# Performance work log

Hardware: AMD Instinct MI355X
Metric: run time of the kernel (lower is better)

## Reference

```python
import jax, jax.numpy as jnp
import numpy as np

C = 512
CR = C // 8  # reduced channels for b/c projections


def setup_inputs() -> dict:
    key = jax.random.key(0)
    ks = jax.random.split(key, 7)
    scale = 1.0 / np.sqrt(C)
    x = jax.random.normal(ks[0], (4, C, 64, 64), dtype=jnp.float32)
    Wb = jax.random.normal(ks[1], (CR, C), dtype=jnp.float32) * scale
    bb = jax.random.normal(ks[2], (CR,), dtype=jnp.float32) * 0.01
    Wc = jax.random.normal(ks[3], (CR, C), dtype=jnp.float32) * scale
    bc = jax.random.normal(ks[4], (CR,), dtype=jnp.float32) * 0.01
    Wd = jax.random.normal(ks[5], (C, C), dtype=jnp.float32) * scale
    bd = jax.random.normal(ks[6], (C,), dtype=jnp.float32) * 0.01
    return {"x": x, "Wb": Wb, "bb": bb, "Wc": Wc, "bc": bc, "Wd": Wd, "bd": bd}


def reference(x, Wb, bb, Wc, bc, Wd, bd):
    B, Cc, H, W = x.shape
    N = H * W
    xf = x.reshape(B, Cc, N)  # [B, C, N] (1x1 conv == per-position matmul)
    b = jnp.einsum('kc,bcn->bkn', Wb, xf) + bb[None, :, None]  # [B, CR, N]
    c = jnp.einsum('kc,bcn->bkn', Wc, xf) + bc[None, :, None]  # [B, CR, N]
    d = jnp.einsum('kc,bcn->bkn', Wd, xf) + bd[None, :, None]  # [B, C, N]
    # s[b,i,j] = sum_k b[b,k,i] * c[b,k,j]; softmax over j
    s = jnp.einsum('bki,bkj->bij', b, c)  # [B, N, N]
    s = jax.nn.softmax(s, axis=-1)
    # torch.bmm(d, s): y[b,c,j] = sum_i d[b,c,i] * s[b,i,j]
    y = jnp.einsum('bci,bij->bcj', d, s)  # [B, C, N]
    return x + y.reshape(B, Cc, H, W)
```

## Files before the change

kernel.cpp:

```cpp
#include <hip/hip_runtime.h>
#include <hip/hip_bf16.h>

typedef float f32x4 __attribute__((ext_vector_type(4)));
typedef float f32x16 __attribute__((ext_vector_type(16)));
typedef short s16x8 __attribute__((ext_vector_type(8)));
typedef uint  u32x4 __attribute__((ext_vector_type(4)));

#define MFMA_BF16(a, b, c) __builtin_amdgcn_mfma_f32_16x16x32_bf16((a), (b), (c), 0, 0, 0)
#define MFMA32(a, b, c)    __builtin_amdgcn_mfma_f32_32x32x16_bf16((a), (b), (c), 0, 0, 0)

__device__ __forceinline__ ushort f2bf(float f) {
  uint u = __builtin_bit_cast(uint, f);
  u += 0x7FFFu + ((u >> 16) & 1u);
  return (ushort)(u >> 16);
}
__device__ __forceinline__ uint pack2bf(float a, float b) {
  return (uint)f2bf(a) | ((uint)f2bf(b) << 16);
}
__device__ __forceinline__ float pexp(float s) {
  float t = fmaf(s, 1.4426950408889634f, -43.2808512266689f);
  float r;
  asm("v_exp_f32 %0, %1" : "=v"(r) : "v"(t));
  return r;
}
__device__ __forceinline__ uint cvtpk(float lo, float hi) {
  uint r;
  asm("v_cvt_pk_bf16_f32 %0, %1, %2" : "=v"(r) : "v"(lo), "v"(hi));
  return r;
}
__device__ __forceinline__ void plswap(uint& a, uint& b) {
  asm("v_permlane32_swap_b32 %0, %1" : "+v"(a), "+v"(b));
}
__device__ __forceinline__ void gld16(const void* g, void* l) {
  __builtin_amdgcn_global_load_lds(
      (const __attribute__((address_space(1))) unsigned int*)g,
      (__attribute__((address_space(3))) unsigned int*)l, 16, 0, 0);
}

#define WS_XT    0UL
#define WS_D     16777216UL
#define WS_BT    33554432UL
#define WS_CT    35651584UL
#define WS_WCAT  37748736UL
#define WS_BCAT  38404096UL
#define WS_E     41943040UL
#define WS_E_NEED (WS_E + 134217728UL)

__global__ void k_prep_w(const float* __restrict__ Wb, const float* __restrict__ bb,
                         const float* __restrict__ Wc, const float* __restrict__ bc,
                         const float* __restrict__ Wd, const float* __restrict__ bd,
                         ushort* __restrict__ Wcat, float* __restrict__ bcat) {
  int idx = blockIdx.x * 256 + threadIdx.x;
  if (idx < 640 * 512) {
    int m = idx >> 9, k = idx & 511;
    float v = (m < 64) ? Wb[m * 512 + k] : (m < 128) ? Wc[(m - 64) * 512 + k] : Wd[(m - 128) * 512 + k];
    Wcat[idx] = f2bf(v);
  }
  if (idx < 640) {
    bcat[idx] = (idx < 64) ? bb[idx] : (idx < 128) ? bc[idx - 64] : bd[idx - 128];
  }
}

__global__ __launch_bounds__(256) void k_prep_xt(const float* __restrict__ x, ushort* __restrict__ xT) {
  __shared__ float tile[64][65];
  int bx = blockIdx.x;
  int b = bx >> 9;
  int c0 = ((bx >> 6) & 7) * 64;
  int n0 = (bx & 63) * 64;
  int t = threadIdx.x;
  const float* xb = x + (size_t)b * 512 * 4096;
#pragma unroll
  for (int p = 0; p < 4; ++p) {
    int cl = (t >> 4) + 16 * p;
    int nf = (t & 15) * 4;
    float4 v = *reinterpret_cast<const float4*>(xb + (size_t)(c0 + cl) * 4096 + n0 + nf);
    tile[cl][nf + 0] = v.x; tile[cl][nf + 1] = v.y; tile[cl][nf + 2] = v.z; tile[cl][nf + 3] = v.w;
  }
  __syncthreads();
  ushort* dst = xT + (size_t)b * 4096 * 512;
#pragma unroll
  for (int q = 0; q < 2; ++q) {
    int ch = t + 256 * q;
    int nl = ch >> 3;
    int cf = (ch & 7) * 8;
    uint4 o;
    o.x = pack2bf(tile[cf + 0][nl], tile[cf + 1][nl]);
    o.y = pack2bf(tile[cf + 2][nl], tile[cf + 3][nl]);
    o.z = pack2bf(tile[cf + 4][nl], tile[cf + 5][nl]);
    o.w = pack2bf(tile[cf + 6][nl], tile[cf + 7][nl]);
    *reinterpret_cast<uint4*>(dst + (size_t)(n0 + nl) * 512 + c0 + cf) = o;
  }
}

__global__ __launch_bounds__(256) void k_proj(const ushort* __restrict__ Wcat, const float* __restrict__ bcat,
                                              const ushort* __restrict__ xT, ushort* __restrict__ bT,
                                              ushort* __restrict__ cT, ushort* __restrict__ dmat) {
  int bx = blockIdx.x;
  int b = bx / 160;
  int r = bx % 160;
  int m0 = (r >> 5) * 128;
  int n0 = (r & 31) * 128;
  int t = threadIdx.x, l = t & 63, w = t >> 6;
  int wm = w >> 1, wn = w & 1, g = l >> 4, l15 = l & 15;
  const ushort* xb = xT + (size_t)b * 4096 * 512;
  f32x4 acc[4][4] = {};
  s16x8 bfn[4];
#pragma unroll
  for (int nt = 0; nt < 4; ++nt)
    bfn[nt] = *reinterpret_cast<const s16x8*>(xb + (size_t)(n0 + 64 * wn + 16 * nt + l15) * 512 + 8 * g);
  for (int k0 = 0; k0 < 512; k0 += 32) {
    s16x8 a[4], bf[4];
#pragma unroll
    for (int nt = 0; nt < 4; ++nt) bf[nt] = bfn[nt];
#pragma unroll
    for (int mt = 0; mt < 4; ++mt)
      a[mt] = *reinterpret_cast<const s16x8*>(Wcat + (size_t)(m0 + 64 * wm + 16 * mt + l15) * 512 + k0 + 8 * g);
    if (k0 + 32 < 512) {
#pragma unroll
      for (int nt = 0; nt < 4; ++nt)
        bfn[nt] = *reinterpret_cast<const s16x8*>(xb + (size_t)(n0 + 64 * wn + 16 * nt + l15) * 512 + k0 + 32 + 8 * g);
    }
    __builtin_amdgcn_sched_barrier(0);
#pragma unroll
    for (int mt = 0; mt < 4; ++mt)
#pragma unroll
      for (int nt = 0; nt < 4; ++nt)
        acc[mt][nt] = MFMA_BF16(a[mt], bf[nt], acc[mt][nt]);
  }
#pragma unroll
  for (int mt = 0; mt < 4; ++mt) {
    int mbase = m0 + 64 * wm + 16 * mt + 4 * g;
#pragma unroll
    for (int nt = 0; nt < 4; ++nt) {
      int n = n0 + 64 * wn + 16 * nt + l15;
      float vv[4];
      vv[0] = acc[mt][nt][0] + bcat[mbase + 0];
      vv[1] = acc[mt][nt][1] + bcat[mbase + 1];
      vv[2] = acc[mt][nt][2] + bcat[mbase + 2];
      vv[3] = acc[mt][nt][3] + bcat[mbase + 3];
      if (mbase < 64) {
        uint2 u2; u2.x = pack2bf(vv[0], vv[1]); u2.y = pack2bf(vv[2], vv[3]);
        size_t off = ((size_t)b * 4096 + n) * 64 + (size_t)((((mbase >> 3) ^ (n & 7)) << 3) + (mbase & 4));
        *reinterpret_cast<uint2*>(bT + off) = u2;
      } else if (mbase < 128) {
        uint2 u2; u2.x = pack2bf(vv[0], vv[1]); u2.y = pack2bf(vv[2], vv[3]);
        *reinterpret_cast<uint2*>(cT + ((size_t)b * 4096 + n) * 64 + (mbase - 64)) = u2;
      } else {
        int cc = mbase - 128;
        size_t fb = (((size_t)b * 256 + (n >> 4)) * 16) * 512;
#pragma unroll
        for (int rr = 0; rr < 4; ++rr) {
          int c = cc + rr;
          size_t idx = fb + (size_t)(c >> 5) * 512 + (size_t)(((n >> 3) & 1) * 32 + (c & 31)) * 8 + (n & 7);
          dmat[idx] = f2bf(vv[rr]);
        }
      }
    }
  }
}

__global__ __launch_bounds__(512) void k_stats_e(const ushort* __restrict__ bT, const ushort* __restrict__ cT,
                                                 ushort* __restrict__ dmat, ushort* __restrict__ E) {
  __shared__ ushort sCT[3][8192];
  __shared__ float lsum[64];
  int bx = blockIdx.x;
  int b = bx >> 6;
  int IC = bx & 63;
  int i0 = IC * 64;
  int t = threadIdx.x, w = t >> 6, l = t & 63;
  int l31 = l & 31, hi = l >> 5;
  int it_s = w & 1, Jl = w >> 1;
  if (t < 64) lsum[t] = 0.f;
  const ushort* bTb = bT + (size_t)b * 262144;
  const ushort* cTb = cT + (size_t)b * 262144;
  int ri = i0 + 32 * it_s + l31;
  int r7 = ri & 7;
  s16x8 af[4];
#pragma unroll
  for (int kc = 0; kc < 4; ++kc)
    af[kc] = *reinterpret_cast<const s16x8*>(bTb + (size_t)ri * 64 + (((2 * kc + hi) ^ r7) << 3));
  __builtin_amdgcn_sched_barrier(0);
  auto STAGE = [&](int st) {
#pragma unroll
    for (int q = 0; q < 2; ++q) {
      int idx = t + 512 * q;
      int row = idx >> 3, u = idx & 7;
      gld16(cTb + (size_t)(st * 128 + row) * 64 + ((u ^ (row & 7)) << 3), &sCT[st % 3][idx * 8]);
    }
  };
  STAGE(0); STAGE(1);
  asm volatile("s_waitcnt vmcnt(2)" ::: "memory");
  __syncthreads();

  f32x16 zero16;
#pragma unroll
  for (int r = 0; r < 16; ++r) zero16[r] = 0.f;
  float lacc[16];
#pragma unroll
  for (int r = 0; r < 16; ++r) lacc[r] = 0.f;

  for (int st = 0; st < 32; ++st) {
    if (st + 2 < 32) STAGE(st + 2);
    __builtin_amdgcn_sched_barrier(0);
    const ushort* cbuf = &sCT[st % 3][0];
    int rj = Jl * 32 + l31;
    int j7 = rj & 7;
    f32x16 sv = zero16;
    __builtin_amdgcn_s_setprio(1);
#pragma unroll
    for (int kc = 0; kc < 4; ++kc) {
      s16x8 cfv = *reinterpret_cast<const s16x8*>(cbuf + rj * 64 + (((2 * kc + hi) ^ j7) << 3));
      sv = MFMA32(af[kc], cfv, sv);
    }
    __builtin_amdgcn_s_setprio(0);
    float p[16];
#pragma unroll
    for (int r = 0; r < 16; ++r) { p[r] = pexp(sv[r]); lacc[r] += p[r]; }
    uint x0 = cvtpk(p[0], p[1]),   y0 = cvtpk(p[4], p[5]);
    uint x1 = cvtpk(p[2], p[3]),   y1 = cvtpk(p[6], p[7]);
    uint x2 = cvtpk(p[8], p[9]),   y2 = cvtpk(p[12], p[13]);
    uint x3 = cvtpk(p[10], p[11]), y3 = cvtpk(p[14], p[15]);
    plswap(x0, y0); plswap(x1, y1); plswap(x2, y2); plswap(x3, y3);
    u32x4 pw0 = {x0, x1, y0, y1};
    u32x4 pw1 = {x2, x3, y2, y3};
    int J = st * 4 + Jl;
    size_t fb = (((size_t)b * 64 + IC) * 128 + J) * 4 + 2 * it_s;
    *reinterpret_cast<u32x4*>(E + (fb * 64 + l) * 8)       = pw0;
    *reinterpret_cast<u32x4*>(E + ((fb + 1) * 64 + l) * 8) = pw1;
    asm volatile("s_waitcnt vmcnt(4)" ::: "memory");
    __builtin_amdgcn_s_barrier();
  }
#pragma unroll
  for (int off = 1; off < 32; off <<= 1)
#pragma unroll
    for (int r = 0; r < 16; ++r) lacc[r] += __shfl_xor(lacc[r], off);
  if (l31 == 0) {
#pragma unroll
    for (int r = 0; r < 16; ++r)
      atomicAdd(&lsum[32 * it_s + (r & 3) + 8 * (r >> 2) + 4 * hi], lacc[r]);
  }
  __syncthreads();
  if (t < 64) lsum[t] = 1.0f / fmaxf(lsum[t], 1e-30f);
  __syncthreads();
  int c = t;
  size_t rowb = (size_t)(c >> 5) * 512 + (size_t)(c & 31) * 8;
#pragma unroll
  for (int q = 0; q < 8; ++q) {
    int ic = (i0 >> 4) + (q >> 1);
    size_t idx = (((size_t)b * 256 + ic) * 16) * 512 + rowb + (size_t)(q & 1) * 256;
    s16x8 v = *reinterpret_cast<s16x8*>(dmat + idx);
    s16x8 nv;
#pragma unroll
    for (int e = 0; e < 8; ++e) {
      float f = __builtin_bit_cast(float, ((uint)(ushort)v[e]) << 16) * lsum[q * 8 + e];
      nv[e] = (short)f2bf(f);
    }
    *reinterpret_cast<s16x8*>(dmat + idx) = nv;
  }
}

__global__ __launch_bounds__(512) void k_attn_e(const ushort* __restrict__ dmat, const ushort* __restrict__ E,
                                                const float* __restrict__ x, float* __restrict__ out) {
  __shared__ ushort sE[3][8192];
  __shared__ ushort sD[3][16384];
  int bid = blockIdx.x;
  int gid = (bid & 7) * 32 + (bid >> 3);
  int b = gid >> 6, jB = (gid >> 1) & 31, cb2 = gid & 1;
  int t = threadIdx.x, w = t >> 6, l = t & 63;
  int l31 = l & 31, hi = l >> 5;
  int cg = w >> 1, jg = w & 1;
  f32x16 zero16;
#pragma unroll
  for (int r = 0; r < 16; ++r) zero16[r] = 0.f;
  f32x16 yacc[2][2];
  yacc[0][0] = zero16; yacc[0][1] = zero16; yacc[1][0] = zero16; yacc[1][1] = zero16;

  auto STAGE = [&](int it) {
    int buf = it % 3;
    const ushort* ebase = E + ((((size_t)b * 64 + it) * 128 + jB * 4) * 4) * 512;
#pragma unroll
    for (int q = 0; q < 2; ++q) {
      int id = t + 512 * q;
      gld16(ebase + (size_t)id * 8, &sE[buf][id * 8]);
    }
#pragma unroll
    for (int q = 0; q < 4; ++q) {
      const ushort* dch = dmat + (((size_t)b * 256 + 4 * it + q) * 16 + cb2 * 8) * 512;
      gld16(dch + (size_t)t * 8, &sD[buf][(q * 512 + t) * 8]);
    }
  };

  STAGE(0); STAGE(1);
  asm volatile("s_waitcnt vmcnt(6)" ::: "memory");
  __builtin_amdgcn_s_barrier();
  __builtin_amdgcn_sched_barrier(0);

  for (int it = 0; it < 64; ++it) {
    if (it + 2 < 64) STAGE(it + 2);
    __builtin_amdgcn_sched_barrier(0);
    const ushort* eb = &sE[it % 3][0];
    const ushort* db = &sD[it % 3][0];
    s16x8 dv[2][4], pfv[2][4];
#pragma unroll
    for (int ch = 0; ch < 4; ++ch) {
#pragma unroll
      for (int ct = 0; ct < 2; ++ct)
        dv[ct][ch] = *reinterpret_cast<const s16x8*>(db + ((ch * 8 + cg * 2 + ct) * 512 + l * 8));
#pragma unroll
      for (int jj = 0; jj < 2; ++jj)
        pfv[jj][ch] = *reinterpret_cast<const s16x8*>(eb + (((jg * 2 + jj) * 4 + ch) * 512 + l * 8));
    }
    __builtin_amdgcn_s_setprio(1);
#pragma unroll
    for (int ch = 0; ch < 4; ++ch) {
#pragma unroll
      for (int ct = 0; ct < 2; ++ct)
#pragma unroll
        for (int jj = 0; jj < 2; ++jj)
          yacc[ct][jj] = MFMA32(dv[ct][ch], pfv[jj][ch], yacc[ct][jj]);
    }
    __builtin_amdgcn_s_setprio(0);
    __builtin_amdgcn_sched_barrier(0);
    if (it < 62) { asm volatile("s_waitcnt vmcnt(6)" ::: "memory"); }
    else         { asm volatile("s_waitcnt vmcnt(0)" ::: "memory"); }
    __builtin_amdgcn_s_barrier();
    __builtin_amdgcn_sched_barrier(0);
  }

#pragma unroll
  for (int ct = 0; ct < 2; ++ct) {
#pragma unroll
    for (int jj = 0; jj < 2; ++jj) {
#pragma unroll
      for (int r = 0; r < 16; ++r) {
        int row = cb2 * 256 + cg * 64 + ct * 32 + (r & 3) + 8 * (r >> 2) + 4 * hi;
        int col = jB * 128 + (jg * 2 + jj) * 32 + l31;
        size_t idx = ((size_t)b * 512 + row) * 4096 + col;
        out[idx] = x[idx] + yacc[ct][jj][r];
      }
    }
  }
}

__global__ __launch_bounds__(512) void k_stats_f(const ushort* __restrict__ bT, const ushort* __restrict__ cT,
                                                 ushort* __restrict__ dmat) {
  __shared__ ushort sCT[3][8192];
  __shared__ float lsum[64];
  int bx = blockIdx.x;
  int b = bx >> 6;
  int i0 = (bx & 63) * 64;
  int t = threadIdx.x, l = t & 63, w = t >> 6;
  int wm = w >> 1, wn = w & 1, g = l >> 4, l15 = l & 15;
  if (t < 64) lsum[t] = 0.f;
  const ushort* bTb = bT + (size_t)b * 262144;
  const ushort* cTb = cT + (size_t)b * 262144;
  int arow = i0 + 16 * wm + l15;
  int r7 = arow & 7;
  const ushort* abase = bTb + (size_t)arow * 64;
  s16x8 a0 = *reinterpret_cast<const s16x8*>(abase + ((g ^ r7) << 3));
  s16x8 a1 = *reinterpret_cast<const s16x8*>(abase + (((g + 4) ^ r7) << 3));
  auto STAGE = [&](int jt) {
#pragma unroll
    for (int q = 0; q < 2; ++q) {
      int idx = t + 512 * q;
      int row = idx >> 3, u = idx & 7;
      gld16(cTb + (size_t)(jt * 128 + row) * 64 + ((u ^ (row & 7)) << 3), &sCT[jt % 3][idx * 8]);
    }
  };
  STAGE(0); STAGE(1);
  asm volatile("s_waitcnt vmcnt(2)" ::: "memory");
  __syncthreads();
  float lacc[4] = {0.f, 0.f, 0.f, 0.f};
  for (int jt = 0; jt < 32; ++jt) {
    if (jt + 2 < 32) STAGE(jt + 2);
    __builtin_amdgcn_sched_barrier(0);
    const ushort* cbuf = &sCT[jt % 3][0];
#pragma unroll
    for (int nt = 0; nt < 4; ++nt) {
      int row = 64 * wn + 16 * nt + l15;
      int rs = row & 7;
      s16x8 b0 = *reinterpret_cast<const s16x8*>(cbuf + row * 64 + ((g ^ rs) << 3));
      s16x8 b1 = *reinterpret_cast<const s16x8*>(cbuf + row * 64 + (((g + 4) ^ rs) << 3));
      f32x4 s = {0.f, 0.f, 0.f, 0.f};
      s = MFMA_BF16(a0, b0, s);
      s = MFMA_BF16(a1, b1, s);
#pragma unroll
      for (int rr = 0; rr < 4; ++rr) lacc[rr] += pexp(s[rr]);
    }
    if (jt < 30) { asm volatile("s_waitcnt vmcnt(2)" ::: "memory"); }
    else         { asm volatile("s_waitcnt vmcnt(0)" ::: "memory"); }
    __builtin_amdgcn_s_barrier();
  }
#pragma unroll
  for (int off = 1; off < 16; off <<= 1)
#pragma unroll
    for (int rr = 0; rr < 4; ++rr) lacc[rr] += __shfl_xor(lacc[rr], off);
  if (l15 == 0) {
#pragma unroll
    for (int rr = 0; rr < 4; ++rr) atomicAdd(&lsum[16 * wm + 4 * g + rr], lacc[rr]);
  }
  __syncthreads();
  if (t < 64) lsum[t] = 1.0f / fmaxf(lsum[t], 1e-30f);
  __syncthreads();
  int c = t;
  size_t rowb = (size_t)(c >> 5) * 512 + (size_t)(c & 31) * 8;
#pragma unroll
  for (int q = 0; q < 8; ++q) {
    int ic = (i0 >> 4) + (q >> 1);
    size_t idx = (((size_t)b * 256 + ic) * 16) * 512 + rowb + (size_t)(q & 1) * 256;
    s16x8 v = *reinterpret_cast<s16x8*>(dmat + idx);
    s16x8 nv;
#pragma unroll
    for (int e = 0; e < 8; ++e) {
      float f = __builtin_bit_cast(float, ((uint)(ushort)v[e]) << 16) * lsum[q * 8 + e];
      nv[e] = (short)f2bf(f);
    }
    *reinterpret_cast<s16x8*>(dmat + idx) = nv;
  }
}

__global__ __launch_bounds__(512, 2) void k_attn_f(const ushort* __restrict__ bT, const ushort* __restrict__ cT,
                                                   const ushort* __restrict__ dmat,
                                                   const float* __restrict__ x, float* __restrict__ out) {
  __shared__ ushort sBT[3][4096];
  __shared__ ushort sP[2][8192];
  int bid = blockIdx.x;
  int gid = (bid & 7) * 64 + (bid >> 3);
  int b   = gid >> 7;
  int cb  = (gid >> 5) & 3;
  int jB  = gid & 31;
  int t = threadIdx.x, w = t >> 6, l = t & 63;
  int l31 = l & 31, hi = l >> 5;
  int it_s = w >> 2, jt_s = w & 3;
  int cg = w >> 1, jg = w & 1;
  const ushort* bTb = bT + (size_t)b * 262144;
  const ushort* cTb = cT + (size_t)b * 262144;
  int js = jB * 128 + jt_s * 32 + l31;
  s16x8 cf[4];
#pragma unroll
  for (int kc = 0; kc < 4; ++kc)
    cf[kc] = *reinterpret_cast<const s16x8*>(cTb + (size_t)js * 64 + kc * 16 + hi * 8);
  int ctg = cb * 4 + cg;
  f32x16 zero16;
#pragma unroll
  for (int r = 0; r < 16; ++r) zero16[r] = 0.f;
  f32x16 yacc[2];
  yacc[0] = zero16; yacc[1] = zero16;
  auto STAGE = [&](int it) {
    gld16(bTb + (size_t)it * 4096 + (size_t)t * 8, &sBT[it % 3][t * 8]);
  };
  STAGE(0); STAGE(1);
  asm volatile("s_waitcnt vmcnt(1)" ::: "memory");
  __builtin_amdgcn_s_barrier();
  __builtin_amdgcn_sched_barrier(0);
  for (int it = 0; it < 64; ++it) {
    s16x8 dv[4];
#pragma unroll
    for (int ch = 0; ch < 4; ++ch)
      dv[ch] = *reinterpret_cast<const s16x8*>(
          dmat + ((((size_t)b * 256 + (4 * it + ch)) * 16 + ctg) * 64 + l) * 8);
    if (it + 2 < 64) STAGE(it + 2);
    __builtin_amdgcn_sched_barrier(0);
    const ushort* bbuf = &sBT[it % 3][0];
    f32x16 sv = zero16;
    __builtin_amdgcn_s_setprio(1);
#pragma unroll
    for (int kc = 0; kc < 4; ++kc) {
      const s16x8 bfv = *reinterpret_cast<const s16x8*>(
          bbuf + (32 * it_s + l31) * 64 + (((2 * kc + hi) ^ (l31 & 7)) << 3));
      sv = MFMA32(bfv, cf[kc], sv);
    }
    __builtin_amdgcn_s_setprio(0);
    float p[16];
#pragma unroll
    for (int r = 0; r < 16; ++r) p[r] = pexp(sv[r]);
    uint x0 = cvtpk(p[0], p[1]),   y0 = cvtpk(p[4], p[5]);
    uint x1 = cvtpk(p[2], p[3]),   y1 = cvtpk(p[6], p[7]);
    uint x2 = cvtpk(p[8], p[9]),   y2 = cvtpk(p[12], p[13]);
    uint x3 = cvtpk(p[10], p[11]), y3 = cvtpk(p[14], p[15]);
    plswap(x0, y0); plswap(x1, y1); plswap(x2, y2); plswap(x3, y3);
    u32x4 pw0 = {x0, x1, y0, y1};
    u32x4 pw1 = {x2, x3, y2, y3};
    ushort* pbuf = &sP[it & 1][0];
    int fi0 = jt_s * 4 + 2 * it_s;
    *reinterpret_cast<s16x8*>(pbuf + (fi0 * 64 + l) * 8)       = __builtin_bit_cast(s16x8, pw0);
    *reinterpret_cast<s16x8*>(pbuf + ((fi0 + 1) * 64 + l) * 8) = __builtin_bit_cast(s16x8, pw1);
    asm volatile("s_waitcnt lgkmcnt(0)" ::: "memory");
    __builtin_amdgcn_s_barrier();
    if (it < 62) { asm volatile("s_waitcnt vmcnt(1)" ::: "memory"); }
    else         { asm volatile("s_waitcnt vmcnt(0)" ::: "memory"); }
    __builtin_amdgcn_sched_barrier(0);
    __builtin_amdgcn_s_setprio(1);
#pragma unroll
    for (int ch = 0; ch < 4; ++ch) {
#pragma unroll
      for (int jj = 0; jj < 2; ++jj) {
        int jt = 2 * jg + jj;
        const s16x8 pfv = *reinterpret_cast<const s16x8*>(pbuf + ((jt * 4 + ch) * 64 + l) * 8);
        yacc[jj] = MFMA32(dv[ch], pfv, yacc[jj]);
      }
    }
    __builtin_amdgcn_s_setprio(0);
  }
#pragma unroll
  for (int jj = 0; jj < 2; ++jj) {
#pragma unroll
    for (int r = 0; r < 16; ++r) {
      int row = cb * 128 + cg * 32 + (r & 3) + 8 * (r >> 2) + 4 * hi;
      int col = jB * 128 + (2 * jg + jj) * 32 + l31;
      size_t idx = ((size_t)b * 512 + row) * 4096 + col;
      out[idx] = x[idx] + yacc[jj][r];
    }
  }
}

extern "C" void kernel_launch(void* const* d_in, const int* in_sizes, int n_in,
                              void* d_out, int out_size, void* d_ws, size_t ws_size,
                              hipStream_t stream) {
  const float* x  = (const float*)d_in[0];
  const float* Wb = (const float*)d_in[1];
  const float* bb = (const float*)d_in[2];
  const float* Wc = (const float*)d_in[3];
  const float* bc = (const float*)d_in[4];
  const float* Wd = (const float*)d_in[5];
  const float* bd = (const float*)d_in[6];
  char* ws = (char*)d_ws;
  ushort* xT   = (ushort*)(ws + WS_XT);
  ushort* dmat = (ushort*)(ws + WS_D);
  ushort* bT   = (ushort*)(ws + WS_BT);
  ushort* cT   = (ushort*)(ws + WS_CT);
  ushort* Wcat = (ushort*)(ws + WS_WCAT);
  float*  bcat = (float*)(ws + WS_BCAT);
  ushort* E    = (ushort*)(ws + WS_E);
  float*  out  = (float*)d_out;

  k_prep_w<<<1280, 256, 0, stream>>>(Wb, bb, Wc, bc, Wd, bd, Wcat, bcat);
  k_prep_xt<<<2048, 256, 0, stream>>>(x, xT);
  k_proj<<<640, 256, 0, stream>>>(Wcat, bcat, xT, bT, cT, dmat);
  if (ws_size >= WS_E_NEED) {
    k_stats_e<<<256, 512, 0, stream>>>(bT, cT, dmat, E);
    k_attn_e<<<256, 512, 0, stream>>>(dmat, E, x, out);
  } else {
    k_stats_f<<<256, 512, 0, stream>>>(bT, cT, dmat);
    k_attn_f<<<512, 512, 0, stream>>>(bT, cT, dmat, x, out);
  }
}
```

Measured before the change: 190.0 us.

## Split attention-apply into 512 smaller blocks with 2-per-CU occupancy

The k_attn_e kernel moves from 256 blocks of 512 threads, each covering 256 output channels, to 512 blocks of 256 threads covering 128 channels, with launch bounds asking for two blocks per CU. The D tile buffer shrinks to double buffering with separate staging for D (one iteration ahead) and E (two ahead), and the vmcnt waits are adjusted to match. The goal is more blocks for the 256 CUs and less LDS per block so two blocks can overlap. In exchange, each E tile is now loaded by twice as many blocks, raising global/L2 traffic for E.

```diff
diff --git a/kernel.cpp b/kernel.cpp
--- a/kernel.cpp
+++ b/kernel.cpp
@@ -259,13 +259,13 @@
   }
 }
 
-__global__ __launch_bounds__(512) void k_attn_e(const ushort* __restrict__ dmat, const ushort* __restrict__ E,
-                                                const float* __restrict__ x, float* __restrict__ out) {
+__global__ __launch_bounds__(256, 2) void k_attn_e(const ushort* __restrict__ dmat, const ushort* __restrict__ E,
+                                                   const float* __restrict__ x, float* __restrict__ out) {
   __shared__ ushort sE[3][8192];
-  __shared__ ushort sD[3][16384];
+  __shared__ ushort sD[2][8192];
   int bid = blockIdx.x;
-  int gid = (bid & 7) * 32 + (bid >> 3);
-  int b = gid >> 6, jB = (gid >> 1) & 31, cb2 = gid & 1;
+  int gid = (bid & 7) * 64 + (bid >> 3);
+  int b = gid >> 7, cb = (gid >> 5) & 3, jB = gid & 31;
   int t = threadIdx.x, w = t >> 6, l = t & 63;
   int l31 = l & 31, hi = l >> 5;
   int cg = w >> 1, jg = w & 1;
@@ -275,40 +275,45 @@
   f32x16 yacc[2][2];
   yacc[0][0] = zero16; yacc[0][1] = zero16; yacc[1][0] = zero16; yacc[1][1] = zero16;
 
-  auto STAGE = [&](int it) {
-    int buf = it % 3;
+  auto STAGE_E = [&](int it) {
     const ushort* ebase = E + ((((size_t)b * 64 + it) * 128 + jB * 4) * 4) * 512;
 #pragma unroll
-    for (int q = 0; q < 2; ++q) {
-      int id = t + 512 * q;
-      gld16(ebase + (size_t)id * 8, &sE[buf][id * 8]);
-    }
-#pragma unroll
     for (int q = 0; q < 4; ++q) {
-      const ushort* dch = dmat + (((size_t)b * 256 + 4 * it + q) * 16 + cb2 * 8) * 512;
-      gld16(dch + (size_t)t * 8, &sD[buf][(q * 512 + t) * 8]);
+      int id = t + 256 * q;
+      gld16(ebase + (size_t)id * 8, &sE[it % 3][id * 8]);
     }
   };
-
-  STAGE(0); STAGE(1);
-  asm volatile("s_waitcnt vmcnt(6)" ::: "memory");
+  auto STAGE_D = [&](int it) {
+    const ushort* dbase = dmat + (((size_t)b * 256 + 4 * it) * 16 + cb * 4) * 512;
+#pragma unroll
+    for (int q = 0; q < 4; ++q) {
+      int id = t + 256 * q;
+      gld16(dbase + (size_t)(id >> 8) * 8192 + (size_t)(id & 255) * 8, &sD[it & 1][id * 8]);
+    }
+  };
+
+  STAGE_E(0);
+  STAGE_D(0);
+  STAGE_E(1);
+  asm volatile("s_waitcnt vmcnt(4)" ::: "memory");
   __builtin_amdgcn_s_barrier();
   __builtin_amdgcn_sched_barrier(0);
 
   for (int it = 0; it < 64; ++it) {
-    if (it + 2 < 64) STAGE(it + 2);
+    if (it + 1 < 64) STAGE_D(it + 1);
+    if (it + 2 < 64) STAGE_E(it + 2);
     __builtin_amdgcn_sched_barrier(0);
     const ushort* eb = &sE[it % 3][0];
-    const ushort* db = &sD[it % 3][0];
+    const ushort* db = &sD[it & 1][0];
     s16x8 dv[2][4], pfv[2][4];
 #pragma unroll
     for (int ch = 0; ch < 4; ++ch) {
 #pragma unroll
       for (int ct = 0; ct < 2; ++ct)
-        dv[ct][ch] = *reinterpret_cast<const s16x8*>(db + ((ch * 8 + cg * 2 + ct) * 512 + l * 8));
+        dv[ct][ch] = *reinterpret_cast<const s16x8*>(db + ((ch * 4 + cg * 2 + ct) * 64 + l) * 8);
 #pragma unroll
       for (int jj = 0; jj < 2; ++jj)
-        pfv[jj][ch] = *reinterpret_cast<const s16x8*>(eb + (((jg * 2 + jj) * 4 + ch) * 512 + l * 8));
+        pfv[jj][ch] = *reinterpret_cast<const s16x8*>(eb + (((jg * 2 + jj) * 4 + ch) * 64 + l) * 8);
     }
     __builtin_amdgcn_s_setprio(1);
 #pragma unroll
@@ -321,19 +326,17 @@
     }
     __builtin_amdgcn_s_setprio(0);
     __builtin_amdgcn_sched_barrier(0);
-    if (it < 62) { asm volatile("s_waitcnt vmcnt(6)" ::: "memory"); }
+    if (it < 62) { asm volatile("s_waitcnt vmcnt(4)" ::: "memory"); }
     else         { asm volatile("s_waitcnt vmcnt(0)" ::: "memory"); }
     __builtin_amdgcn_s_barrier();
-    __builtin_amdgcn_sched_barrier(0);
-  }
-
+  }
 #pragma unroll
   for (int ct = 0; ct < 2; ++ct) {
 #pragma unroll
     for (int jj = 0; jj < 2; ++jj) {
 #pragma unroll
       for (int r = 0; r < 16; ++r) {
-        int row = cb2 * 256 + cg * 64 + ct * 32 + (r & 3) + 8 * (r >> 2) + 4 * hi;
+        int row = cb * 128 + cg * 64 + ct * 32 + (r & 3) + 8 * (r >> 2) + 4 * hi;
         int col = jB * 128 + (jg * 2 + jj) * 32 + l31;
         size_t idx = ((size_t)b * 512 + row) * 4096 + col;
         out[idx] = x[idx] + yacc[ct][jj][r];
@@ -539,7 +542,7 @@
   k_proj<<<640, 256, 0, stream>>>(Wcat, bcat, xT, bT, cT, dmat);
   if (ws_size >= WS_E_NEED) {
     k_stats_e<<<256, 512, 0, stream>>>(bT, cT, dmat, E);
-    k_attn_e<<<256, 512, 0, stream>>>(dmat, E, x, out);
+    k_attn_e<<<512, 256, 0, stream>>>(dmat, E, x, out);
   } else {
     k_stats_f<<<256, 512, 0, stream>>>(bT, cT, dmat);
     k_attn_f<<<512, 512, 0, stream>>>(bT, cT, dmat, x, out);
```

Result: no change. 190.8 us (+0.4%).
